# Kernel optimization log

Hardware: AMD Instinct MI355X
Metric: run time of the kernel (lower is better)

The kernel has to match this reference:

```python
import jax, jax.numpy as jnp
import numpy as np
import math

B, S, D = 2, 2048, 2048
H, KVH, HD = 32, 4, 64  # n_heads, n_kv_heads, head_dim
ROPE_THETA = 10000.0


def apply_rope(t, cos, sin):
    # t: (B, S, h, HD); cos/sin: (S, HD//2)
    tr = t.reshape(*t.shape[:-1], HD // 2, 2)
    xr, xi = tr[..., 0], tr[..., 1]
    c = cos[None, :, None, :]
    s = sin[None, :, None, :]
    out_r = xr * c - xi * s
    out_i = xr * s + xi * c
    return jnp.stack([out_r, out_i], axis=-1).reshape(t.shape)


def setup_inputs() -> dict:
    key = jax.random.key(0)
    ks = jax.random.split(key, 6)
    x = jax.random.normal(ks[0], (B, S, D), dtype=jnp.float32)
    # weights stored as (in, out); Linear(in,out,bias=False) is x @ W
    sc = lambda fan_in: 1.0 / math.sqrt(fan_in)
    wq = jax.random.normal(ks[1], (D, H * HD), dtype=jnp.float32) * sc(D)
    wk = jax.random.normal(ks[2], (D, KVH * HD), dtype=jnp.float32) * sc(D)
    wv = jax.random.normal(ks[3], (D, KVH * HD), dtype=jnp.float32) * sc(D)
    wo = jax.random.normal(ks[4], (H * HD, D), dtype=jnp.float32) * sc(H * HD)
    # precompute rotary cos/sin: angles[t, j] = t / theta^(2j/HD)
    inv_freq = 1.0 / (ROPE_THETA ** (np.arange(0, HD, 2, dtype=np.float32) / HD))
    t = np.arange(S, dtype=np.float32)
    angles = np.outer(t, inv_freq)  # (S, HD//2)
    freqs_cis = jnp.asarray(np.stack([np.cos(angles), np.sin(angles)], axis=-1))  # (S, HD//2, 2)
    # causal additive mask
    neg_inf = jnp.float32(-1e9)
    mask = jnp.where(jnp.arange(S)[None, :] > jnp.arange(S)[:, None], neg_inf, 0.0).astype(jnp.float32)
    return {"x": x, "freqs_cis": freqs_cis, "mask": mask, "wq": wq, "wk": wk, "wv": wv, "wo": wo}


def reference(x, freqs_cis, mask, wq, wk, wv, wo):
    bsz, seqlen, _ = x.shape
    cos, sin = freqs_cis[..., 0], freqs_cis[..., 1]
    xq = (x @ wq).reshape(bsz, seqlen, H, HD)
    xk = (x @ wk).reshape(bsz, seqlen, KVH, HD)
    xv = (x @ wv).reshape(bsz, seqlen, KVH, HD)
    xq = apply_rope(xq, cos, sin)
    xk = apply_rope(xk, cos, sin)
    # GQA expand: each kv head repeated n_rep times consecutively
    n_rep = H // KVH
    keys = jnp.repeat(xk, n_rep, axis=2)    # (B, S, H, HD)
    values = jnp.repeat(xv, n_rep, axis=2)  # (B, S, H, HD)
    q = xq.transpose(0, 2, 1, 3)      # (B, H, S, HD)
    k = keys.transpose(0, 2, 1, 3)
    v = values.transpose(0, 2, 1, 3)
    scores = jnp.einsum("bhqd,bhkd->bhqk", q, k) / math.sqrt(HD)
    scores = scores + mask[None, None, :, :]
    probs = jax.nn.softmax(scores.astype(jnp.float32), axis=-1).astype(q.dtype)
    out = jnp.einsum("bhqk,bhkd->bhqd", probs, v)
    out = out.transpose(0, 2, 1, 3).reshape(bsz, seqlen, H * HD)
    return out @ wo
```

## Files before the change

kernel.cpp:

```cpp
#include <hip/hip_runtime.h>
#include <hip/hip_bf16.h>
#include <stdint.h>

#define B_    2
#define S_    2048
#define D_    2048
#define H_    32
#define KVH_  4
#define HD_   64
#define QKVN  2560

typedef __bf16 bf16_t;
typedef __bf16 bf16x8 __attribute__((ext_vector_type(8)));
typedef __bf16 bf16x4 __attribute__((ext_vector_type(4)));
typedef __bf16 bf16x2 __attribute__((ext_vector_type(2)));
typedef float  f32x4  __attribute__((ext_vector_type(4)));

#define MFMA16(a, b, c) __builtin_amdgcn_mfma_f32_16x16x32_bf16(a, b, c, 0, 0, 0)

__device__ __forceinline__ void gld16(const void* g, void* l) {
  __builtin_amdgcn_global_load_lds(
      (const __attribute__((address_space(1))) uint32_t*)(uintptr_t)g,
      (__attribute__((address_space(3))) uint32_t*)(uint32_t)(uintptr_t)l,
      16, 0, 0);
}

__global__ __launch_bounds__(256) void cvt_bf16_k(const float* __restrict__ in,
                                                  bf16_t* __restrict__ out, int n4) {
  int i = blockIdx.x * 256 + threadIdx.x;
  if (i >= n4) return;
  float4 v = ((const float4*)in)[i];
  bf16x4 o = { (bf16_t)v.x, (bf16_t)v.y, (bf16_t)v.z, (bf16_t)v.w };
  ((bf16x4*)out)[i] = o;
}

__global__ __launch_bounds__(256) void transpose_cvt_k(const float* __restrict__ src,
                                                       bf16_t* __restrict__ dst,
                                                       int K, int N) {
  __shared__ float tile[32][33];
  int kb = blockIdx.x * 32, nb = blockIdx.y * 32;
  int tx = threadIdx.x & 31, ty = threadIdx.x >> 5;
  #pragma unroll
  for (int i = ty; i < 32; i += 8)
    tile[i][tx] = src[(long)(kb + i) * N + (nb + tx)];
  __syncthreads();
  #pragma unroll
  for (int i = ty; i < 32; i += 8)
    dst[(long)(nb + i) * K + (kb + tx)] = (bf16_t)tile[tx][i];
}

__global__ __launch_bounds__(256) void gemm128_k(const bf16_t* __restrict__ A,
                                                 const bf16_t* __restrict__ Bt,
                                                 float* __restrict__ C,
                                                 int M, int N, int K) {
  __shared__ bf16_t As[128 * 32];
  __shared__ bf16_t Bs[128 * 32];
  const int tid = threadIdx.x, lane = tid & 63;
  const int wave = tid >> 6, wr = wave >> 1, wc = wave & 1;
  const int lrow = lane & 15, quad = lane >> 4;
  const long m0 = (long)blockIdx.x * 128, n0 = (long)blockIdx.y * 128;

  f32x4 acc[4][4];
  #pragma unroll
  for (int i = 0; i < 4; i++)
    #pragma unroll
    for (int j = 0; j < 4; j++) acc[i][j] = (f32x4){0.f, 0.f, 0.f, 0.f};

  const int r0 = tid >> 2;
  const int cg = ((tid & 3) ^ (r0 & 3)) * 8;
  const bf16_t* Ag0 = A  + (m0 + r0) * (long)K + cg;
  const bf16_t* Ag1 = Ag0 + 64 * (long)K;
  const bf16_t* Bg0 = Bt + (n0 + r0) * (long)K + cg;
  const bf16_t* Bg1 = Bg0 + 64 * (long)K;
  bf16_t* As0 = As + tid * 8; bf16_t* As1 = As0 + 2048;
  bf16_t* Bs0 = Bs + tid * 8; bf16_t* Bs1 = Bs0 + 2048;
  const int swz = (quad ^ (lrow & 3)) * 8;

  for (int k0 = 0; k0 < K; k0 += 32) {
    gld16(Ag0 + k0, As0);
    gld16(Ag1 + k0, As1);
    gld16(Bg0 + k0, Bs0);
    gld16(Bg1 + k0, Bs1);
    __syncthreads();
    bf16x8 af[4], bfr[4];
    #pragma unroll
    for (int i = 0; i < 4; i++)
      af[i] = *(const bf16x8*)&As[(wr * 64 + i * 16 + lrow) * 32 + swz];
    #pragma unroll
    for (int j = 0; j < 4; j++)
      bfr[j] = *(const bf16x8*)&Bs[(wc * 64 + j * 16 + lrow) * 32 + swz];
    #pragma unroll
    for (int i = 0; i < 4; i++)
      #pragma unroll
      for (int j = 0; j < 4; j++)
        acc[i][j] = MFMA16(af[i], bfr[j], acc[i][j]);
    __syncthreads();
  }

  #pragma unroll
  for (int i = 0; i < 4; i++) {
    #pragma unroll
    for (int r = 0; r < 4; r++) {
      long row = m0 + wr * 64 + i * 16 + quad * 4 + r;
      float* cp = C + row * N + n0 + wc * 64 + lrow;
      #pragma unroll
      for (int j = 0; j < 4; j++) cp[j * 16] = acc[i][j][r];
    }
  }
}

__global__ __launch_bounds__(256) void ropepack_k(const float* __restrict__ QKV,
                                                  const float* __restrict__ freqs,
                                                  bf16_t* __restrict__ Qb,
                                                  bf16_t* __restrict__ Kb) {
  const int PAIRS = (H_ + KVH_) * (HD_ / 2);
  int idx = blockIdx.x * 256 + threadIdx.x;
  int row = idx / PAIRS;
  int p   = idx % PAIRS;
  if (row >= B_ * S_) return;
  int s    = row & (S_ - 1);
  int b    = row >> 11;
  int head = p >> 5;
  int j    = p & 31;
  float2 f = ((const float2*)freqs)[s * 32 + j];
  int col = (head < H_) ? (head * HD_ + 2 * j)
                        : (D_ + (head - H_) * HD_ + 2 * j);
  float2 v = *(const float2*)&QKV[(long)row * QKVN + col];
  float2 o = { v.x * f.x - v.y * f.y, v.x * f.y + v.y * f.x };
  if (head < H_) {
    const float qs = 0.125f * 1.4426950408889634f;
    o.x *= qs; o.y *= qs;
    bf16x2 w = { (bf16_t)o.x, (bf16_t)o.y };
    *(bf16x2*)&Qb[(((long)(b * H_ + head) * S_ + s) * HD_) + 2 * j] = w;
  } else {
    bf16x2 w = { (bf16_t)o.x, (bf16_t)o.y };
    *(bf16x2*)&Kb[(((long)(b * KVH_ + (head - H_)) * S_ + s) * HD_) + 2 * j] = w;
  }
}

__global__ __launch_bounds__(256) void vtrans_k(const float* __restrict__ QKV,
                                                bf16_t* __restrict__ Vt) {
  __shared__ float tile[32][33];
  int s0 = blockIdx.x * 32, d0 = blockIdx.y * 32, bkv = blockIdx.z;
  int b = bkv >> 2, kv = bkv & 3;
  int tx = threadIdx.x & 31, ty = threadIdx.x >> 5;
  const float* src = QKV + (long)b * S_ * QKVN + D_ + KVH_ * HD_ + kv * HD_;
  #pragma unroll
  for (int i = ty; i < 32; i += 8)
    tile[i][tx] = src[(long)(s0 + i) * QKVN + d0 + tx];
  __syncthreads();
  #pragma unroll
  for (int i = ty; i < 32; i += 8)
    Vt[((long)bkv * HD_ + d0 + i) * S_ + s0 + tx] = (bf16_t)tile[tx][i];
}

__global__ __launch_bounds__(256) void fattn_k(const bf16_t* __restrict__ Qb,
                                               const bf16_t* __restrict__ Kb,
                                               const bf16_t* __restrict__ Vt,
                                               bf16_t* __restrict__ attnb) {
  __shared__ bf16_t KQs[64 * 64];
  __shared__ bf16_t Vts[64 * 64];
  __shared__ bf16_t Pt[4][16 * 64];

  const int qt = (S_ / 64 - 1) - blockIdx.x;
  const int q0 = qt * 64;
  const int bh = blockIdx.y;
  const int b = bh >> 5, h = bh & (H_ - 1), kv = h >> 3;
  const int tid = threadIdx.x, wave = tid >> 6, lane = tid & 63;
  const int lrow = lane & 15, quad = lane >> 4;
  const int qw = q0 + wave * 16;

  const bf16_t* Qg = Qb + ((long)bh * S_ + q0) * HD_;
  const bf16_t* Kg = Kb + (long)(b * KVH_ + kv) * S_ * HD_;
  const bf16_t* Vg = Vt + (long)(b * KVH_ + kv) * HD_ * S_;

  const int sr  = tid >> 3;
  const int scg = ((tid & 7) ^ (sr & 7)) * 8;
  const long qkoff0 = (long)sr * HD_ + scg;
  const long qkoff1 = (long)(sr + 32) * HD_ + scg;
  const long voff0  = (long)sr * S_ + scg;
  const long voff1  = (long)(sr + 32) * S_ + scg;
  bf16_t* lds_lo = KQs + tid * 8;
  bf16_t* lds_hi = KQs + 2048 + tid * 8;
  bf16_t* vlds_lo = Vts + tid * 8;
  bf16_t* vlds_hi = Vts + 2048 + tid * 8;

  gld16(Qg + qkoff0, lds_lo);
  gld16(Qg + qkoff1, lds_hi);
  __syncthreads();
  const int sw0 = (quad ^ (lrow & 7)) * 8;
  const int sw1 = sw0 ^ 32;
  bf16x8 bq0 = *(const bf16x8*)&KQs[(wave * 16 + lrow) * 64 + sw0];
  bf16x8 bq1 = *(const bf16x8*)&KQs[(wave * 16 + lrow) * 64 + sw1];
  __syncthreads();

  f32x4 o[4];
  #pragma unroll
  for (int db = 0; db < 4; db++) o[db] = (f32x4){0.f, 0.f, 0.f, 0.f};
  float lp = 0.f;

  bf16_t* PtW = &Pt[wave][0];
  const int prow = lrow * 64;

  const int nt = qt + 1;
  for (int t = 0; t < nt; t++) {
    const long k0 = (long)t * 64;
    gld16(Kg + k0 * HD_ + qkoff0, lds_lo);
    gld16(Kg + k0 * HD_ + qkoff1, lds_hi);
    gld16(Vg + k0 + voff0, vlds_lo);
    gld16(Vg + k0 + voff1, vlds_hi);
    __syncthreads();

    f32x4 s[4];
    #pragma unroll
    for (int kb = 0; kb < 4; kb++) {
      const int kbase = (int)k0 + kb * 16;
      if (kbase <= qw) {
        bf16x8 ak0 = *(const bf16x8*)&KQs[(kb * 16 + lrow) * 64 + sw0];
        bf16x8 ak1 = *(const bf16x8*)&KQs[(kb * 16 + lrow) * 64 + sw1];
        f32x4 sv = {0.f, 0.f, 0.f, 0.f};
        sv = MFMA16(ak0, bq0, sv);
        sv = MFMA16(ak1, bq1, sv);
        if (kbase == qw) {
          #pragma unroll
          for (int r = 0; r < 4; r++)
            if (quad * 4 + r > lrow) sv[r] = -1e30f;
        }
        s[kb] = sv;
      } else {
        s[kb] = (f32x4){-1e30f, -1e30f, -1e30f, -1e30f};
      }
    }

    #pragma unroll
    for (int kb = 0; kb < 4; kb++) {
      bf16x4 pw;
      #pragma unroll
      for (int r = 0; r < 4; r++) {
        float p = exp2f(s[kb][r]);
        lp += p;
        pw[r] = (bf16_t)p;
      }
      const int chunk = kb * 2 + (quad >> 1);
      *(bf16x4*)&PtW[prow + ((chunk ^ (lrow & 7)) * 8) + (quad & 1) * 4] = pw;
    }
    bf16x8 bp0 = *(const bf16x8*)&PtW[prow + ((quad ^ (lrow & 7)) * 8)];
    bf16x8 bp1 = *(const bf16x8*)&PtW[prow + (((4 + quad) ^ (lrow & 7)) * 8)];
    #pragma unroll
    for (int db = 0; db < 4; db++) {
      bf16x8 av0 = *(const bf16x8*)&Vts[(db * 16 + lrow) * 64 + sw0];
      bf16x8 av1 = *(const bf16x8*)&Vts[(db * 16 + lrow) * 64 + sw1];
      o[db] = MFMA16(av0, bp0, o[db]);
      o[db] = MFMA16(av1, bp1, o[db]);
    }
    __syncthreads();
  }

  float l = lp;
  l += __shfl_xor(l, 16, 64);
  l += __shfl_xor(l, 32, 64);
  const float inv = 1.f / l;
  const int query = qw + lrow;
  bf16_t* op = attnb + ((long)(b * S_ + query)) * D_ + h * HD_;
  #pragma unroll
  for (int db = 0; db < 4; db++) {
    bf16x4 w = { (bf16_t)(o[db][0] * inv), (bf16_t)(o[db][1] * inv),
                 (bf16_t)(o[db][2] * inv), (bf16_t)(o[db][3] * inv) };
    *(bf16x4*)&op[db * 16 + quad * 4] = w;
  }
}

extern "C" void kernel_launch(void* const* d_in, const int* in_sizes, int n_in,
                              void* d_out, int out_size, void* d_ws, size_t ws_size,
                              hipStream_t stream) {
  const float* x     = (const float*)d_in[0];
  const float* freqs = (const float*)d_in[1];
  const float* wq    = (const float*)d_in[3];
  const float* wk    = (const float*)d_in[4];
  const float* wv    = (const float*)d_in[5];
  const float* wo    = (const float*)d_in[6];
  float* out = (float*)d_out;

  char* ws = (char*)d_ws;
  bf16_t* xb    = (bf16_t*)(ws);
  bf16_t* wcat  = (bf16_t*)(ws + 16777216);
  bf16_t* woT   = (bf16_t*)(ws + 27262976);
  float*  QKV   = (float*) (ws + 35651584);
  bf16_t* Qb    = xb;
  bf16_t* Kb    = (bf16_t*)(ws + 16777216);
  bf16_t* Vt    = (bf16_t*)(ws + 18874368);
  bf16_t* attnb = (bf16_t*)(ws + 35651584);

  cvt_bf16_k<<<8192, 256, 0, stream>>>(x, xb, 2097152);

  { dim3 g(64, 64); transpose_cvt_k<<<g, 256, 0, stream>>>(wq, wcat, 2048, 2048); }
  { dim3 g(64, 8);
    transpose_cvt_k<<<g, 256, 0, stream>>>(wk, wcat + (long)2048 * 2048, 2048, 256);
    transpose_cvt_k<<<g, 256, 0, stream>>>(wv, wcat + (long)2304 * 2048, 2048, 256); }
  { dim3 g(64, 64); transpose_cvt_k<<<g, 256, 0, stream>>>(wo, woT, 2048, 2048); }

  { dim3 g(32, 20); gemm128_k<<<g, 256, 0, stream>>>(xb, wcat, QKV, 4096, QKVN, 2048); }

  ropepack_k<<<18432, 256, 0, stream>>>(QKV, freqs, Qb, Kb);
  { dim3 g(64, 2, 8); vtrans_k<<<g, 256, 0, stream>>>(QKV, Vt); }

  { dim3 g(32, 64); fattn_k<<<g, 256, 0, stream>>>(Qb, Kb, Vt, attnb); }

  { dim3 g(32, 16); gemm128_k<<<g, 256, 0, stream>>>(attnb, woT, out, 4096, 2048, 2048); }
}
```

Baseline: 412.9 us.

## Process two GQA query heads per attention block to share K/V tiles

Each flash-attention block now handles two query heads that share the same KV head, loading each K/V tile into LDS once and running both heads' score and PV MFMAs against it. This halves the K/V global loads and barriers per unit of work and halves the grid size. In exchange it uses more registers and LDS, and fully masked sub-tiles now write explicit zeros to the P buffer. Fewer blocks may reduce occupancy and parallelism on the causal-imbalanced grid.

```diff
diff --git a/kernel.cpp b/kernel.cpp
--- a/kernel.cpp
+++ b/kernel.cpp
@@ -160,17 +160,17 @@
                                                bf16_t* __restrict__ attnb) {
   __shared__ bf16_t KQs[64 * 64];
   __shared__ bf16_t Vts[64 * 64];
-  __shared__ bf16_t Pt[4][16 * 64];
+  __shared__ bf16_t Pt[8][16 * 64];
 
   const int qt = (S_ / 64 - 1) - blockIdx.x;
   const int q0 = qt * 64;
-  const int bh = blockIdx.y;
-  const int b = bh >> 5, h = bh & (H_ - 1), kv = h >> 3;
+  const int pi = blockIdx.y;
+  const int b = pi >> 4, kv = (pi >> 2) & 3, e = pi & 3;
+  const int h0 = kv * 8 + e * 2;
   const int tid = threadIdx.x, wave = tid >> 6, lane = tid & 63;
   const int lrow = lane & 15, quad = lane >> 4;
   const int qw = q0 + wave * 16;
 
-  const bf16_t* Qg = Qb + ((long)bh * S_ + q0) * HD_;
   const bf16_t* Kg = Kb + (long)(b * KVH_ + kv) * S_ * HD_;
   const bf16_t* Vg = Vt + (long)(b * KVH_ + kv) * HD_ * S_;
 
@@ -185,21 +185,30 @@
   bf16_t* vlds_lo = Vts + tid * 8;
   bf16_t* vlds_hi = Vts + 2048 + tid * 8;
 
-  gld16(Qg + qkoff0, lds_lo);
-  gld16(Qg + qkoff1, lds_hi);
-  __syncthreads();
   const int sw0 = (quad ^ (lrow & 7)) * 8;
   const int sw1 = sw0 ^ 32;
-  bf16x8 bq0 = *(const bf16x8*)&KQs[(wave * 16 + lrow) * 64 + sw0];
-  bf16x8 bq1 = *(const bf16x8*)&KQs[(wave * 16 + lrow) * 64 + sw1];
-  __syncthreads();
-
-  f32x4 o[4];
-  #pragma unroll
-  for (int db = 0; db < 4; db++) o[db] = (f32x4){0.f, 0.f, 0.f, 0.f};
-  float lp = 0.f;
-
-  bf16_t* PtW = &Pt[wave][0];
+
+  bf16x8 bq[2][2];
+  #pragma unroll
+  for (int hh = 0; hh < 2; hh++) {
+    const bf16_t* Qg = Qb + ((long)((b * H_ + h0 + hh) * S_) + q0) * HD_;
+    gld16(Qg + qkoff0, lds_lo);
+    gld16(Qg + qkoff1, lds_hi);
+    __syncthreads();
+    bq[hh][0] = *(const bf16x8*)&KQs[(wave * 16 + lrow) * 64 + sw0];
+    bq[hh][1] = *(const bf16x8*)&KQs[(wave * 16 + lrow) * 64 + sw1];
+    __syncthreads();
+  }
+
+  f32x4 o[2][4];
+  #pragma unroll
+  for (int hh = 0; hh < 2; hh++)
+    #pragma unroll
+    for (int db = 0; db < 4; db++) o[hh][db] = (f32x4){0.f, 0.f, 0.f, 0.f};
+  float lp[2] = {0.f, 0.f};
+
+  bf16_t* PtW0 = &Pt[wave * 2 + 0][0];
+  bf16_t* PtW1 = &Pt[wave * 2 + 1][0];
   const int prow = lrow * 64;
 
   const int nt = qt + 1;
@@ -211,62 +220,86 @@
     gld16(Vg + k0 + voff1, vlds_hi);
     __syncthreads();
 
-    f32x4 s[4];
+    f32x4 s[2][4];
     #pragma unroll
     for (int kb = 0; kb < 4; kb++) {
       const int kbase = (int)k0 + kb * 16;
       if (kbase <= qw) {
         bf16x8 ak0 = *(const bf16x8*)&KQs[(kb * 16 + lrow) * 64 + sw0];
         bf16x8 ak1 = *(const bf16x8*)&KQs[(kb * 16 + lrow) * 64 + sw1];
-        f32x4 sv = {0.f, 0.f, 0.f, 0.f};
-        sv = MFMA16(ak0, bq0, sv);
-        sv = MFMA16(ak1, bq1, sv);
-        if (kbase == qw) {
+        #pragma unroll
+        for (int hh = 0; hh < 2; hh++) {
+          f32x4 sv = {0.f, 0.f, 0.f, 0.f};
+          sv = MFMA16(ak0, bq[hh][0], sv);
+          sv = MFMA16(ak1, bq[hh][1], sv);
+          if (kbase == qw) {
+            #pragma unroll
+            for (int r = 0; r < 4; r++)
+              if (quad * 4 + r > lrow) sv[r] = -1e30f;
+          }
+          s[hh][kb] = sv;
+        }
+      } else {
+        s[0][kb] = (f32x4){-2e30f, -2e30f, -2e30f, -2e30f};
+        s[1][kb] = (f32x4){-2e30f, -2e30f, -2e30f, -2e30f};
+      }
+    }
+
+    #pragma unroll
+    for (int kb = 0; kb < 4; kb++) {
+      const int kbase = (int)k0 + kb * 16;
+      const int pcol = (((kb * 2 + (quad >> 1)) ^ (lrow & 7)) * 8) + (quad & 1) * 4;
+      if (kbase <= qw) {
+        #pragma unroll
+        for (int hh = 0; hh < 2; hh++) {
+          bf16x4 pw;
           #pragma unroll
-          for (int r = 0; r < 4; r++)
-            if (quad * 4 + r > lrow) sv[r] = -1e30f;
+          for (int r = 0; r < 4; r++) {
+            float p = exp2f(s[hh][kb][r]);
+            lp[hh] += p;
+            pw[r] = (bf16_t)p;
+          }
+          *(bf16x4*)&((hh ? PtW1 : PtW0)[prow + pcol]) = pw;
         }
-        s[kb] = sv;
       } else {
-        s[kb] = (f32x4){-1e30f, -1e30f, -1e30f, -1e30f};
+        bf16x4 z = {(bf16_t)0.f, (bf16_t)0.f, (bf16_t)0.f, (bf16_t)0.f};
+        *(bf16x4*)&PtW0[prow + pcol] = z;
+        *(bf16x4*)&PtW1[prow + pcol] = z;
       }
     }
 
-    #pragma unroll
-    for (int kb = 0; kb < 4; kb++) {
-      bf16x4 pw;
-      #pragma unroll
-      for (int r = 0; r < 4; r++) {
-        float p = exp2f(s[kb][r]);
-        lp += p;
-        pw[r] = (bf16_t)p;
-      }
-      const int chunk = kb * 2 + (quad >> 1);
-      *(bf16x4*)&PtW[prow + ((chunk ^ (lrow & 7)) * 8) + (quad & 1) * 4] = pw;
-    }
-    bf16x8 bp0 = *(const bf16x8*)&PtW[prow + ((quad ^ (lrow & 7)) * 8)];
-    bf16x8 bp1 = *(const bf16x8*)&PtW[prow + (((4 + quad) ^ (lrow & 7)) * 8)];
+    bf16x8 bp[2][2];
+    bp[0][0] = *(const bf16x8*)&PtW0[prow + ((quad ^ (lrow & 7)) * 8)];
+    bp[0][1] = *(const bf16x8*)&PtW0[prow + (((4 + quad) ^ (lrow & 7)) * 8)];
+    bp[1][0] = *(const bf16x8*)&PtW1[prow + ((quad ^ (lrow & 7)) * 8)];
+    bp[1][1] = *(const bf16x8*)&PtW1[prow + (((4 + quad) ^ (lrow & 7)) * 8)];
     #pragma unroll
     for (int db = 0; db < 4; db++) {
       bf16x8 av0 = *(const bf16x8*)&Vts[(db * 16 + lrow) * 64 + sw0];
       bf16x8 av1 = *(const bf16x8*)&Vts[(db * 16 + lrow) * 64 + sw1];
-      o[db] = MFMA16(av0, bp0, o[db]);
-      o[db] = MFMA16(av1, bp1, o[db]);
-    }
-    __syncthreads();
-  }
-
-  float l = lp;
-  l += __shfl_xor(l, 16, 64);
-  l += __shfl_xor(l, 32, 64);
-  const float inv = 1.f / l;
+      #pragma unroll
+      for (int hh = 0; hh < 2; hh++) {
+        o[hh][db] = MFMA16(av0, bp[hh][0], o[hh][db]);
+        o[hh][db] = MFMA16(av1, bp[hh][1], o[hh][db]);
+      }
+    }
+    __syncthreads();
+  }
+
   const int query = qw + lrow;
-  bf16_t* op = attnb + ((long)(b * S_ + query)) * D_ + h * HD_;
-  #pragma unroll
-  for (int db = 0; db < 4; db++) {
-    bf16x4 w = { (bf16_t)(o[db][0] * inv), (bf16_t)(o[db][1] * inv),
-                 (bf16_t)(o[db][2] * inv), (bf16_t)(o[db][3] * inv) };
-    *(bf16x4*)&op[db * 16 + quad * 4] = w;
+  #pragma unroll
+  for (int hh = 0; hh < 2; hh++) {
+    float l = lp[hh];
+    l += __shfl_xor(l, 16, 64);
+    l += __shfl_xor(l, 32, 64);
+    const float inv = 1.f / l;
+    bf16_t* op = attnb + ((long)(b * S_ + query)) * D_ + (h0 + hh) * HD_;
+    #pragma unroll
+    for (int db = 0; db < 4; db++) {
+      bf16x4 w = { (bf16_t)(o[hh][db][0] * inv), (bf16_t)(o[hh][db][1] * inv),
+                   (bf16_t)(o[hh][db][2] * inv), (bf16_t)(o[hh][db][3] * inv) };
+      *(bf16x4*)&op[db * 16 + quad * 4] = w;
+    }
   }
 }
 
@@ -304,7 +337,7 @@
   ropepack_k<<<18432, 256, 0, stream>>>(QKV, freqs, Qb, Kb);
   { dim3 g(64, 2, 8); vtrans_k<<<g, 256, 0, stream>>>(QKV, Vt); }
 
-  { dim3 g(32, 64); fattn_k<<<g, 256, 0, stream>>>(Qb, Kb, Vt, attnb); }
+  { dim3 g(32, 32); fattn_k<<<g, 256, 0, stream>>>(Qb, Kb, Vt, attnb); }
 
   { dim3 g(32, 16); gemm128_k<<<g, 256, 0, stream>>>(attnb, woT, out, 4096, 2048, 2048); }
 }
```

After: 423.3 us. 1.03x slower.
